# Performance work log

Measured on AMD Instinct MI355X. Metric: run time of the kernel, lower is better.

The kernel has to match this reference:

```python
import jax, jax.numpy as jnp
import numpy as np

WINDOW = 15          # kornia disk heatmap_to_keypoints window_size
THRESH = 0.99        # score_threshold
K = 1024             # fixed number of NMS keypoints kept per image (top-K padding of variable count)
EPS = 1e-12          # F.normalize eps


def setup_inputs() -> dict:
    key = jax.random.key(0)
    k1, k2 = jax.random.split(key)
    B, C, H, W = 4, 129, 512, 512
    J = 512
    input_tensor = jax.random.normal(k1, (B, C, H, W), dtype=jnp.float32)
    juncs_pred_hawp = jax.random.randint(k2, (B, J, 2), 0, 512, dtype=jnp.int32)
    return {"input_tensor": input_tensor, "juncs_pred_hawp": juncs_pred_hawp}


def reference(input_tensor, juncs_pred_hawp):
    B, C, H, W = input_tensor.shape
    heatmap = input_tensor[:, 0]          # [B,H,W]
    fmap = input_tensor[:, 1:129]         # [B,128,H,W]

    # --- window NMS (15x15 local max + threshold), as in kornia.feature.disk.detector.nms ---
    pooled = jax.lax.reduce_window(heatmap, -jnp.inf, jax.lax.max,
                                   (1, WINDOW, WINDOW), (1, 1, 1), 'SAME')
    nms_mask = (heatmap == pooled) & (heatmap > THRESH)   # [B,H,W]

    # --- fixed-K top-k over NMS survivors (padded equivalent of variable-count nonzero) ---
    flat = heatmap.reshape(B, H * W)
    masked = jnp.where(nms_mask.reshape(B, H * W), flat, -jnp.inf)
    kp_logp, kp_idx = jax.lax.top_k(masked, K)            # [B,K] each
    y = kp_idx // W
    x = kp_idx % W
    kp_xy = jnp.stack([x, y], axis=-1).astype(jnp.int32)  # [B,K,2] in (x,y) order

    # --- concat HAWP junctions (cast to int) with NMS keypoints ---
    keypoints_final = jnp.concatenate([juncs_pred_hawp.astype(jnp.int32), kp_xy], axis=1)  # [B,J+K,2]

    # --- per-batch descriptor gather at (y,x), then L2 normalize (F.normalize dim=-1) ---
    xk = keypoints_final[..., 0]
    yk = keypoints_final[..., 1]
    flat_idx = yk * W + xk                                 # [B,N]
    fmap_flat = fmap.reshape(B, 128, H * W)
    desc = jnp.take_along_axis(fmap_flat, flat_idx[:, None, :], axis=2)  # [B,128,N]
    desc = jnp.swapaxes(desc, 1, 2)                        # [B,N,128]
    norm = jnp.maximum(jnp.linalg.norm(desc, axis=-1, keepdims=True), EPS)
    desc = desc / norm

    # --- scores: detection logp of NMS keypoints normalized by per-image max; ones for junctions ---
    scores_kp = kp_logp / jnp.max(kp_logp, axis=-1, keepdims=True)       # [B,K]
    J = juncs_pred_hawp.shape[1]
    scores = jnp.concatenate([jnp.ones((B, J), dtype=desc.dtype), scores_kp], axis=-1)  # [B,J+K]

    return keypoints_final, desc, scores
```

## Files before the change

### kernel.cpp

```cpp
#include <hip/hip_runtime.h>
#include <math.h>
#include <stdint.h>

#define BB 4
#define CC 129
#define HH 512
#define WW 512
#define HWSZ (HH*WW)
#define JJ 512
#define KK 1024
#define NKP (JJ+KK)
#define RAD 7
#define TS 32
#define HL (TS + 2*RAD)
#define TPB 256
#define SLOTS 32
#define NL 2048
#define NMS_THRESH 0.99f
#define SENT 0xFF800000FFFFFFFFULL

static const size_t OFF_TCNT  = 0;
static const size_t OFF_TKEYS = 4096;

__global__ __launch_bounds__(256)
void k_nms(const float* __restrict__ in, int* __restrict__ tileCnt,
           uint64_t* __restrict__ tileKeys) {
    __shared__ float s[HL*HL];
    __shared__ float hm[HL*TS];
    __shared__ int tcnt;
    const int tid = threadIdx.x, blk = blockIdx.x;
    int b = blk >> 8, t = blk & 255;
    int ty = t >> 4, tx = t & 15;
    int by = ty*TS - RAD, bx = tx*TS - RAD;
    const float* heat = in + (size_t)b * CC * HWSZ;
    if (tid == 0) tcnt = 0;
    for (int i = tid; i < HL*HL; i += 256) {
        int r = i / HL, c = i - r*HL;
        int gy = by + r, gx = bx + c;
        s[i] = (gy >= 0 && gy < HH && gx >= 0 && gx < WW)
                 ? heat[gy*WW + gx] : -INFINITY;
    }
    __syncthreads();
    for (int i = tid; i < HL*TS; i += 256) {
        int r = i >> 5, c = i & 31;
        const float* sp = s + r*HL + c;
        float m = sp[0];
        #pragma unroll
        for (int k = 1; k < 15; ++k) m = fmaxf(m, sp[k]);
        hm[i] = m;
    }
    __syncthreads();
    uint64_t* tk = tileKeys + (size_t)blk * SLOTS;
    for (int i = tid; i < TS*TS; i += 256) {
        int r = i >> 5, c = i & 31;
        float v = s[(r+RAD)*HL + (c+RAD)];
        if (v > NMS_THRESH) {
            const float* hp = hm + r*TS + c;
            float m = hp[0];
            #pragma unroll
            for (int k = 1; k < 15; ++k) m = fmaxf(m, hp[k*TS]);
            if (v == m) {
                int pos = atomicAdd(&tcnt, 1);
                if (pos < SLOTS) {
                    uint32_t idx = (uint32_t)((ty*TS + r)*WW + (tx*TS + c));
                    tk[pos] = ((uint64_t)__float_as_uint(v) << 32)
                            | (uint32_t)(~idx);
                }
            }
        }
    }
    __syncthreads();
    if (tid == 0) tileCnt[blk] = (tcnt < SLOTS) ? tcnt : SLOTS;
}

__global__ __launch_bounds__(256)
void k_rankdesc(const float* __restrict__ in, const int* __restrict__ juncs,
                const int* __restrict__ tileCnt, const uint64_t* __restrict__ tileKeys,
                float* __restrict__ out_kp, float* __restrict__ out_desc,
                float* __restrict__ out_sc) {
    __shared__ uint64_t sk[NL];
    __shared__ int sca[TPB], scb[TPB];
    __shared__ int part[256];
    __shared__ float red[256];
    __shared__ uint64_t eKey[16];
    __shared__ int eRank[16];
    const int tid = threadIdx.x, blk = blockIdx.x;

    {
        int w = tid >> 6, l = tid & 63;
        int j = blk*4 + w;
        int jb = j >> 9, jk = j & 511;
        int kx = juncs[(jb*JJ + jk)*2 + 0];
        int ky = juncs[(jb*JJ + jk)*2 + 1];
        int fi = ky*WW + kx;
        const float* fp = in + (size_t)jb*CC*HWSZ + HWSZ + fi;
        float a0 = fp[(size_t)l*HWSZ];
        float a1 = fp[(size_t)(l + 64)*HWSZ];
        float sq = a0*a0 + a1*a1;
        for (int m = 1; m < 64; m <<= 1) sq += __shfl_xor(sq, m, 64);
        float nrm = fmaxf(sqrtf(sq), 1e-12f);
        int go = jb*NKP + jk;
        float* dp = out_desc + (size_t)go * 128;
        dp[l]      = a0 / nrm;
        dp[l + 64] = a1 / nrm;
        if (l == 0) {
            out_kp[2*go]     = (float)kx;
            out_kp[2*go + 1] = (float)ky;
            out_sc[go]       = 1.0f;
        }
    }

    int b = blk >> 7, chunk = blk & 127;
    int i0 = chunk * 16;
    int cnt_t = tileCnt[b*TPB + tid];
    sca[tid] = cnt_t;
    __syncthreads();
    int* src = sca; int* dst = scb;
    for (int off = 1; off < TPB; off <<= 1) {
        dst[tid] = src[tid] + ((tid >= off) ? src[tid - off] : 0);
        __syncthreads();
        int* tmp = src; src = dst; dst = tmp;
    }
    int off_t = src[tid] - cnt_t;
    int n = src[TPB-1]; if (n > NL) n = NL;
    const uint64_t* tkb = tileKeys + (size_t)(b*TPB) * SLOTS;
    for (int j = 0; j < cnt_t; ++j) {
        int o = off_t + j;
        if (o < NL) sk[o] = tkb[(size_t)tid*SLOTS + j];
    }
    __syncthreads();

    float mx = -INFINITY;
    for (int i = tid; i < n; i += 256)
        mx = fmaxf(mx, __uint_as_float((uint32_t)(sk[i] >> 32)));
    red[tid] = mx;
    __syncthreads();
    for (int s2 = 128; s2 > 0; s2 >>= 1) {
        if (tid < s2) red[tid] = fmaxf(red[tid], red[tid + s2]);
        __syncthreads();
    }
    float v0 = red[0];

    {
        int it = tid & 15, sub = tid >> 4;
        int i = i0 + it;
        uint64_t key = (i < n) ? sk[i] : SENT;
        int jc = (n + 15) >> 4;
        int j0 = sub*jc, j1 = j0 + jc; if (j1 > n) j1 = n;
        int r = 0;
        for (int j = j0; j < j1; ++j) r += (sk[j] > key);
        part[tid] = r;
        __syncthreads();
        if (tid < 16) {
            int rank = 0;
            #pragma unroll
            for (int s2 = 0; s2 < 16; ++s2) rank += part[s2*16 + tid];
            int i_ = i0 + tid;
            if (i_ >= n) rank = i_;
            eKey[tid]  = (i_ < n) ? sk[i_] : SENT;
            eRank[tid] = rank;
        }
        __syncthreads();
    }

    {
        int hw = tid >> 5, l = tid & 31;
        for (int s2 = hw; s2 < 16; s2 += 8) {
            int rank = eRank[s2];
            if (rank < KK) {
                uint64_t key = eKey[s2];
                float v = __uint_as_float((uint32_t)(key >> 32));
                int rr = (int)(~(uint32_t)key);
                int kx = rr & (WW-1), ky = (rr >> 9) & (HH-1);
                float sc = v / v0;
                int fi = ky*WW + kx;
                const float* fp = in + (size_t)b*CC*HWSZ + HWSZ + fi;
                float a0 = fp[(size_t)(l      )*HWSZ];
                float a1 = fp[(size_t)(l + 32 )*HWSZ];
                float a2 = fp[(size_t)(l + 64 )*HWSZ];
                float a3 = fp[(size_t)(l + 96 )*HWSZ];
                float sq = a0*a0 + a1*a1 + a2*a2 + a3*a3;
                for (int m = 1; m < 32; m <<= 1) sq += __shfl_xor(sq, m, 32);
                float nrm = fmaxf(sqrtf(sq), 1e-12f);
                int go = b*NKP + JJ + rank;
                float* dp = out_desc + (size_t)go * 128;
                dp[l]      = a0 / nrm;
                dp[l + 32] = a1 / nrm;
                dp[l + 64] = a2 / nrm;
                dp[l + 96] = a3 / nrm;
                if (l == 0) {
                    out_kp[2*go]     = (float)kx;
                    out_kp[2*go + 1] = (float)ky;
                    out_sc[go]       = sc;
                }
            }
        }
    }
}

extern "C" void kernel_launch(void* const* d_in, const int* in_sizes, int n_in,
                              void* d_out, int out_size, void* d_ws, size_t ws_size,
                              hipStream_t stream) {
    const float* in  = (const float*)d_in[0];
    const int* juncs = (const int*)d_in[1];
    float* out       = (float*)d_out;

    char* ws = (char*)d_ws;
    int*      tileCnt  = (int*)(ws + OFF_TCNT);
    uint64_t* tileKeys = (uint64_t*)(ws + OFF_TKEYS);

    float* out_kp   = out;
    float* out_desc = out + (size_t)BB*NKP*2;
    float* out_sc   = out + (size_t)BB*NKP*2 + (size_t)BB*NKP*128;

    k_nms     <<<BB*TPB, 256, 0, stream>>>(in, tileCnt, tileKeys);
    k_rankdesc<<<512,    256, 0, stream>>>(in, juncs, tileCnt, tileKeys,
                                           out_kp, out_desc, out_sc);
}
```

Before: 37.74 us.

## Move junction descriptors into NMS kernel and prefetch keypoint features before ranking

The junction descriptor gather moves out of the rank kernel into 256 extra blocks of the NMS kernel, so it runs alongside the heatmap NMS instead of on the critical path after it. In the rank kernel, each half-wave loads the feature vectors of its candidate keypoints right after the keys are staged in shared memory, ahead of the max and rank computation, so the gather latency overlaps with the ranking. The tree max reduction becomes a wavefront shuffle plus a 4-entry combine, and a barrier phase is removed. The cost is extra speculative loads for candidates that end up outside the top K.

```diff
diff --git a/kernel.cpp b/kernel.cpp
--- a/kernel.cpp
+++ b/kernel.cpp
@@ -17,19 +17,53 @@
 #define SLOTS 32
 #define NL 2048
 #define NMS_THRESH 0.99f
+#define JDB 256
 #define SENT 0xFF800000FFFFFFFFULL
 
 static const size_t OFF_TCNT  = 0;
 static const size_t OFF_TKEYS = 4096;
 
 __global__ __launch_bounds__(256)
-void k_nms(const float* __restrict__ in, int* __restrict__ tileCnt,
-           uint64_t* __restrict__ tileKeys) {
+void k_nms(const float* __restrict__ in, const int* __restrict__ juncs,
+           int* __restrict__ tileCnt, uint64_t* __restrict__ tileKeys,
+           float* __restrict__ out_kp, float* __restrict__ out_desc,
+           float* __restrict__ out_sc) {
     __shared__ float s[HL*HL];
     __shared__ float hm[HL*TS];
     __shared__ int tcnt;
     const int tid = threadIdx.x, blk = blockIdx.x;
-    int b = blk >> 8, t = blk & 255;
+
+    if (blk < JDB) {
+        int g2 = tid >> 5, l = tid & 31;
+        int j  = blk*8 + g2;
+        int jb = j >> 9, jk = j & 511;
+        int kx = juncs[(jb*JJ + jk)*2 + 0];
+        int ky = juncs[(jb*JJ + jk)*2 + 1];
+        int fi = ky*WW + kx;
+        const float* fp = in + (size_t)jb*CC*HWSZ + HWSZ + fi;
+        float a0 = fp[(size_t)(l      )*HWSZ];
+        float a1 = fp[(size_t)(l + 32 )*HWSZ];
+        float a2 = fp[(size_t)(l + 64 )*HWSZ];
+        float a3 = fp[(size_t)(l + 96 )*HWSZ];
+        float sq = a0*a0 + a1*a1 + a2*a2 + a3*a3;
+        for (int m = 1; m < 32; m <<= 1) sq += __shfl_xor(sq, m, 32);
+        float nrm = fmaxf(sqrtf(sq), 1e-12f);
+        int go = jb*NKP + jk;
+        float* dp = out_desc + (size_t)go * 128;
+        dp[l]      = a0 / nrm;
+        dp[l + 32] = a1 / nrm;
+        dp[l + 64] = a2 / nrm;
+        dp[l + 96] = a3 / nrm;
+        if (l == 0) {
+            out_kp[2*go]     = (float)kx;
+            out_kp[2*go + 1] = (float)ky;
+            out_sc[go]       = 1.0f;
+        }
+        return;
+    }
+
+    int blk2 = blk - JDB;
+    int b = blk2 >> 8, t = blk2 & 255;
     int ty = t >> 4, tx = t & 15;
     int by = ty*TS - RAD, bx = tx*TS - RAD;
     const float* heat = in + (size_t)b * CC * HWSZ;
@@ -50,7 +84,7 @@
         hm[i] = m;
     }
     __syncthreads();
-    uint64_t* tk = tileKeys + (size_t)blk * SLOTS;
+    uint64_t* tk = tileKeys + (size_t)blk2 * SLOTS;
     for (int i = tid; i < TS*TS; i += 256) {
         int r = i >> 5, c = i & 31;
         float v = s[(r+RAD)*HL + (c+RAD)];
@@ -70,48 +104,22 @@
         }
     }
     __syncthreads();
-    if (tid == 0) tileCnt[blk] = (tcnt < SLOTS) ? tcnt : SLOTS;
+    if (tid == 0) tileCnt[blk2] = (tcnt < SLOTS) ? tcnt : SLOTS;
 }
 
 __global__ __launch_bounds__(256)
-void k_rankdesc(const float* __restrict__ in, const int* __restrict__ juncs,
+void k_rankdesc(const float* __restrict__ in,
                 const int* __restrict__ tileCnt, const uint64_t* __restrict__ tileKeys,
                 float* __restrict__ out_kp, float* __restrict__ out_desc,
                 float* __restrict__ out_sc) {
     __shared__ uint64_t sk[NL];
     __shared__ int sca[TPB], scb[TPB];
     __shared__ int part[256];
-    __shared__ float red[256];
-    __shared__ uint64_t eKey[16];
-    __shared__ int eRank[16];
+    __shared__ float wmax[4];
     const int tid = threadIdx.x, blk = blockIdx.x;
-
-    {
-        int w = tid >> 6, l = tid & 63;
-        int j = blk*4 + w;
-        int jb = j >> 9, jk = j & 511;
-        int kx = juncs[(jb*JJ + jk)*2 + 0];
-        int ky = juncs[(jb*JJ + jk)*2 + 1];
-        int fi = ky*WW + kx;
-        const float* fp = in + (size_t)jb*CC*HWSZ + HWSZ + fi;
-        float a0 = fp[(size_t)l*HWSZ];
-        float a1 = fp[(size_t)(l + 64)*HWSZ];
-        float sq = a0*a0 + a1*a1;
-        for (int m = 1; m < 64; m <<= 1) sq += __shfl_xor(sq, m, 64);
-        float nrm = fmaxf(sqrtf(sq), 1e-12f);
-        int go = jb*NKP + jk;
-        float* dp = out_desc + (size_t)go * 128;
-        dp[l]      = a0 / nrm;
-        dp[l + 64] = a1 / nrm;
-        if (l == 0) {
-            out_kp[2*go]     = (float)kx;
-            out_kp[2*go + 1] = (float)ky;
-            out_sc[go]       = 1.0f;
-        }
-    }
-
     int b = blk >> 7, chunk = blk & 127;
     int i0 = chunk * 16;
+
     int cnt_t = tileCnt[b*TPB + tid];
     sca[tid] = cnt_t;
     __syncthreads();
@@ -130,69 +138,72 @@
     }
     __syncthreads();
 
+    const int hw = tid >> 5, l = tid & 31;
+    const int sA = hw, sB = hw + 8;
+    uint64_t keyA = (i0 + sA < n) ? sk[i0 + sA] : SENT;
+    uint64_t keyB = (i0 + sB < n) ? sk[i0 + sB] : SENT;
+    int idxA = (int)(~(uint32_t)keyA) & (HWSZ-1);
+    int idxB = (int)(~(uint32_t)keyB) & (HWSZ-1);
+    const float* fbase = in + (size_t)b*CC*HWSZ + HWSZ;
+    const float* fpA = fbase + idxA;
+    const float* fpB = fbase + idxB;
+    float a0 = fpA[(size_t)(l      )*HWSZ];
+    float a1 = fpA[(size_t)(l + 32 )*HWSZ];
+    float a2 = fpA[(size_t)(l + 64 )*HWSZ];
+    float a3 = fpA[(size_t)(l + 96 )*HWSZ];
+    float b0 = fpB[(size_t)(l      )*HWSZ];
+    float b1 = fpB[(size_t)(l + 32 )*HWSZ];
+    float b2 = fpB[(size_t)(l + 64 )*HWSZ];
+    float b3 = fpB[(size_t)(l + 96 )*HWSZ];
+
     float mx = -INFINITY;
     for (int i = tid; i < n; i += 256)
         mx = fmaxf(mx, __uint_as_float((uint32_t)(sk[i] >> 32)));
-    red[tid] = mx;
-    __syncthreads();
-    for (int s2 = 128; s2 > 0; s2 >>= 1) {
-        if (tid < s2) red[tid] = fmaxf(red[tid], red[tid + s2]);
-        __syncthreads();
-    }
-    float v0 = red[0];
+    for (int m = 1; m < 64; m <<= 1) mx = fmaxf(mx, __shfl_xor(mx, m, 64));
+    if ((tid & 63) == 0) wmax[tid >> 6] = mx;
 
     {
         int it = tid & 15, sub = tid >> 4;
-        int i = i0 + it;
-        uint64_t key = (i < n) ? sk[i] : SENT;
+        uint64_t key = (i0 + it < n) ? sk[i0 + it] : SENT;
         int jc = (n + 15) >> 4;
         int j0 = sub*jc, j1 = j0 + jc; if (j1 > n) j1 = n;
         int r = 0;
         for (int j = j0; j < j1; ++j) r += (sk[j] > key);
         part[tid] = r;
-        __syncthreads();
-        if (tid < 16) {
-            int rank = 0;
+    }
+    __syncthreads();
+    float v0 = fmaxf(fmaxf(wmax[0], wmax[1]), fmaxf(wmax[2], wmax[3]));
+
+    #pragma unroll
+    for (int pick = 0; pick < 2; ++pick) {
+        int s2 = pick ? sB : sA;
+        uint64_t key = pick ? keyB : keyA;
+        float c0 = pick ? b0 : a0, c1 = pick ? b1 : a1;
+        float c2 = pick ? b2 : a2, c3 = pick ? b3 : a3;
+        int i_ = i0 + s2;
+        int rank;
+        if (i_ < n) {
+            rank = 0;
             #pragma unroll
-            for (int s2 = 0; s2 < 16; ++s2) rank += part[s2*16 + tid];
-            int i_ = i0 + tid;
-            if (i_ >= n) rank = i_;
-            eKey[tid]  = (i_ < n) ? sk[i_] : SENT;
-            eRank[tid] = rank;
-        }
-        __syncthreads();
-    }
-
-    {
-        int hw = tid >> 5, l = tid & 31;
-        for (int s2 = hw; s2 < 16; s2 += 8) {
-            int rank = eRank[s2];
-            if (rank < KK) {
-                uint64_t key = eKey[s2];
-                float v = __uint_as_float((uint32_t)(key >> 32));
-                int rr = (int)(~(uint32_t)key);
-                int kx = rr & (WW-1), ky = (rr >> 9) & (HH-1);
-                float sc = v / v0;
-                int fi = ky*WW + kx;
-                const float* fp = in + (size_t)b*CC*HWSZ + HWSZ + fi;
-                float a0 = fp[(size_t)(l      )*HWSZ];
-                float a1 = fp[(size_t)(l + 32 )*HWSZ];
-                float a2 = fp[(size_t)(l + 64 )*HWSZ];
-                float a3 = fp[(size_t)(l + 96 )*HWSZ];
-                float sq = a0*a0 + a1*a1 + a2*a2 + a3*a3;
-                for (int m = 1; m < 32; m <<= 1) sq += __shfl_xor(sq, m, 32);
-                float nrm = fmaxf(sqrtf(sq), 1e-12f);
-                int go = b*NKP + JJ + rank;
-                float* dp = out_desc + (size_t)go * 128;
-                dp[l]      = a0 / nrm;
-                dp[l + 32] = a1 / nrm;
-                dp[l + 64] = a2 / nrm;
-                dp[l + 96] = a3 / nrm;
-                if (l == 0) {
-                    out_kp[2*go]     = (float)kx;
-                    out_kp[2*go + 1] = (float)ky;
-                    out_sc[go]       = sc;
-                }
+            for (int q = 0; q < 16; ++q) rank += part[q*16 + s2];
+        } else rank = i_;
+        if (rank < KK) {
+            float v = __uint_as_float((uint32_t)(key >> 32));
+            int rr = (int)(~(uint32_t)key);
+            int kx = rr & (WW-1), ky = (rr >> 9) & (HH-1);
+            float sq = c0*c0 + c1*c1 + c2*c2 + c3*c3;
+            for (int m = 1; m < 32; m <<= 1) sq += __shfl_xor(sq, m, 32);
+            float nrm = fmaxf(sqrtf(sq), 1e-12f);
+            int go = b*NKP + JJ + rank;
+            float* dp = out_desc + (size_t)go * 128;
+            dp[l]      = c0 / nrm;
+            dp[l + 32] = c1 / nrm;
+            dp[l + 64] = c2 / nrm;
+            dp[l + 96] = c3 / nrm;
+            if (l == 0) {
+                out_kp[2*go]     = (float)kx;
+                out_kp[2*go + 1] = (float)ky;
+                out_sc[go]       = v / v0;
             }
         }
     }
@@ -213,7 +224,8 @@
     float* out_desc = out + (size_t)BB*NKP*2;
     float* out_sc   = out + (size_t)BB*NKP*2 + (size_t)BB*NKP*128;
 
-    k_nms     <<<BB*TPB, 256, 0, stream>>>(in, tileCnt, tileKeys);
-    k_rankdesc<<<512,    256, 0, stream>>>(in, juncs, tileCnt, tileKeys,
-                                           out_kp, out_desc, out_sc);
+    k_nms     <<<JDB + BB*TPB, 256, 0, stream>>>(in, juncs, tileCnt, tileKeys,
+                                                 out_kp, out_desc, out_sc);
+    k_rankdesc<<<512,          256, 0, stream>>>(in, tileCnt, tileKeys,
+                                                 out_kp, out_desc, out_sc);
 }
```

After: 38.62 us, median of 2. 1.02x slower.
